# Performance work log

Measured on AMD Instinct MI355X. Metric: run time of the kernel, lower is better.

## Reference

```python
import jax, jax.numpy as jnp
import numpy as np

B, S, H = 2, 1024, 1024
NH, NKV, HD = 16, 4, 64
E, TOPK, I = 8, 2, 3584
EPS = 1e-5
THETA = 1e6


def setup_inputs() -> dict:
    key = jax.random.key(0)
    ks = jax.random.split(key, 12)
    def w(k, shape, fan_in):
        return jax.random.normal(k, shape, dtype=jnp.float32) * (1.0 / np.sqrt(fan_in))
    return {
        "hidden_states": jax.random.normal(ks[0], (B, S, H), dtype=jnp.float32),
        "position_ids": jnp.broadcast_to(jnp.arange(S, dtype=jnp.int64)[None, :], (B, S)),
        "ln1_w": jnp.ones((H,), jnp.float32),
        "ln2_w": jnp.ones((H,), jnp.float32),
        "wq": w(ks[1], (H, NH * HD), H),
        "wk": w(ks[2], (H, NKV * HD), H),
        "wv": w(ks[3], (H, NKV * HD), H),
        "wo": w(ks[4], (NH * HD, H), NH * HD),
        "router_w": w(ks[5], (H, E), H),
        "w_gate": w(ks[6], (E, H, I), H),
        "w_up": w(ks[7], (E, H, I), H),
        "w_down": w(ks[8], (E, I, H), I),
    }


def _rmsnorm(x, w):
    xf = x.astype(jnp.float32)
    return (xf * jax.lax.rsqrt(jnp.mean(xf * xf, -1, keepdims=True) + EPS)).astype(x.dtype) * w


def _rope(x, pos):
    # x: [B,S,nh,HD], pos: [B,S]
    inv_freq = 1.0 / (THETA ** (jnp.arange(0, HD, 2, dtype=jnp.float32) / HD))
    ang = pos.astype(jnp.float32)[..., None] * inv_freq            # [B,S,HD/2]
    emb = jnp.concatenate([ang, ang], axis=-1)                      # [B,S,HD]
    cos, sin = jnp.cos(emb)[:, :, None, :], jnp.sin(emb)[:, :, None, :]
    x1, x2 = x[..., : HD // 2], x[..., HD // 2:]
    rot = jnp.concatenate([-x2, x1], axis=-1)
    return x * cos + rot * sin


def _forward(hidden_states, position_ids, ln1_w, ln2_w, wq, wk, wv, wo,
             router_w, w_gate, w_up, w_down):
    residual = hidden_states
    x = _rmsnorm(hidden_states, ln1_w)

    # ---- attention (GQA, causal, RoPE) ----
    q = (x @ wq).reshape(B, S, NH, HD)
    k = (x @ wk).reshape(B, S, NKV, HD)
    v = (x @ wv).reshape(B, S, NKV, HD)
    q = _rope(q, position_ids)
    k = _rope(k, position_ids)
    rep = NH // NKV
    k = jnp.repeat(k, rep, axis=2)  # [B,S,NH,HD]
    v = jnp.repeat(v, rep, axis=2)
    scores = jnp.einsum("bqhd,bkhd->bhqk", q, k) / np.sqrt(HD)
    causal = jnp.tril(jnp.ones((S, S), bool))
    scores = jnp.where(causal[None, None], scores, jnp.finfo(scores.dtype).min)
    probs = jax.nn.softmax(scores, axis=-1)
    attn = jnp.einsum("bhqk,bkhd->bqhd", probs, v).reshape(B, S, NH * HD)
    hidden = residual + attn @ wo

    # ---- MoE MLP ----
    residual = hidden
    xn = _rmsnorm(hidden, ln2_w).reshape(-1, H)               # [T,H]
    T = xn.shape[0]
    logits = xn @ router_w                                    # [T,E]
    rprobs = jax.nn.softmax(logits.astype(jnp.float32), axis=-1)
    topv, topi = jax.lax.top_k(rprobs, TOPK)                  # [T,TOPK]
    topv = topv / jnp.sum(topv, axis=-1, keepdims=True)       # normalize_top_k_affinities
    weights = jnp.zeros((T, E), jnp.float32).at[jnp.arange(T)[:, None], topi].set(topv)
    g = jnp.einsum("th,ehi->eti", xn, w_gate)                 # [E,T,I]
    u = jnp.einsum("th,ehi->eti", xn, w_up)
    a = jax.nn.silu(g) * u
    eo = jnp.einsum("eti,eih->eth", a, w_down)                # [E,T,H]
    moe = jnp.einsum("eth,te->th", eo, weights).reshape(B, S, H)
    return residual + moe


def reference(hidden_states, position_ids, ln1_w, ln2_w, wq, wk, wv, wo,
              router_w, w_gate, w_up, w_down):
    return _forward(hidden_states, position_ids, ln1_w, ln2_w, wq, wk, wv, wo,
                    router_w, w_gate, w_up, w_down)
```

## Files before the change

### kernel.cpp

```cpp
#include <hip/hip_runtime.h>
#include <hip/hip_bf16.h>
#include <math.h>

#define Bc 2
#define Sc 1024
#define Hc 1024
#define NHc 16
#define NKVc 4
#define HDc 64
#define Ec 8
#define TOPKc 2
#define Ic 3584
#define Tc (Bc*Sc)
#define EPSc 1e-5f

typedef __attribute__((ext_vector_type(8))) short bf16x8;
typedef __attribute__((ext_vector_type(4))) float f32x4;

__device__ __forceinline__ unsigned short f2bf(float f) {
    union { float f; unsigned u; } v; v.f = f;
    unsigned r = v.u + 0x7fffu + ((v.u >> 16) & 1u);
    return (unsigned short)(r >> 16);
}

__device__ __forceinline__ unsigned cvt_pk_bf16(float lo, float hi) {
    unsigned r;
    asm("v_cvt_pk_bf16_f32 %0, %1, %2" : "=v"(r) : "v"(lo), "v"(hi));
    return r;
}

#define GLL(g, l) __builtin_amdgcn_global_load_lds( \
    (const __attribute__((address_space(1))) void*)(g), \
    (__attribute__((address_space(3))) void*)(l), 16, 0, 0)

static const size_t OFF_XN1  = 0;
static const size_t OFF_QB   = 8*1024*1024;
static const size_t OFF_KB   = OFF_QB + 8*1024*1024;
static const size_t OFF_VB   = OFF_KB + 2*1024*1024;
static const size_t OFF_XN2F = OFF_VB + 2*1024*1024;
static const size_t OFF_XN2B = OFF_XN2F + 8*1024*1024;
static const size_t OFF_ACT  = OFF_XN2B + 4*1024*1024;
static const size_t OFF_ROUTE= OFF_ACT + (size_t)4096*3584*2;

__global__ __launch_bounds__(256) void rmsnorm_kernel(const float* __restrict__ x,
        const float* __restrict__ w, float* __restrict__ outf,
        unsigned short* __restrict__ outb) {
    int t = blockIdx.x;
    int tid = threadIdx.x;
    const float* row = x + (size_t)t * Hc;
    float ss = 0.f;
    for (int h = tid; h < Hc; h += 256) { float v = row[h]; ss += v*v; }
    __shared__ float red[256];
    red[tid] = ss; __syncthreads();
    for (int s = 128; s > 0; s >>= 1) { if (tid < s) red[tid] += red[tid+s]; __syncthreads(); }
    float scale = rsqrtf(red[0] / (float)Hc + EPSc);
    for (int h = tid; h < Hc; h += 256) {
        float v = row[h] * scale * w[h];
        outf[(size_t)t*Hc + h] = v;
        if (outb) outb[(size_t)t*Hc + h] = f2bf(v);
    }
}

__global__ __launch_bounds__(256) void qkv_gemm(const float* __restrict__ A,
        const float* __restrict__ wq, const float* __restrict__ wk, const float* __restrict__ wv,
        float* __restrict__ qout, float* __restrict__ kout, float* __restrict__ vout) {
    __shared__ float As[64][17];
    __shared__ float Bs[16][65];
    int n0 = blockIdx.x * 64;
    int m0 = blockIdx.y * 64;
    int tid = threadIdx.x;
    int tx = tid & 15, ty = tid >> 4;
    const float* Bp; int ldb, c0;
    if (n0 < 1024)      { Bp = wq; ldb = 1024; c0 = n0; }
    else if (n0 < 1280) { Bp = wk; ldb = 256;  c0 = n0 - 1024; }
    else                { Bp = wv; ldb = 256;  c0 = n0 - 1280; }
    float acc[4][4] = {};
    for (int k0 = 0; k0 < 1024; k0 += 16) {
        #pragma unroll
        for (int i = 0; i < 4; i++) {
            int lin = tid + i*256; int r = lin >> 4, k = lin & 15;
            As[r][k] = A[(size_t)(m0 + r)*Hc + k0 + k];
        }
        #pragma unroll
        for (int i = 0; i < 4; i++) {
            int lin = tid + i*256; int r = lin >> 6, c = lin & 63;
            Bs[r][c] = Bp[(size_t)(k0 + r)*ldb + c0 + c];
        }
        __syncthreads();
        #pragma unroll
        for (int kk = 0; kk < 16; kk++) {
            float a[4], b[4];
            #pragma unroll
            for (int i = 0; i < 4; i++) a[i] = As[ty*4+i][kk];
            #pragma unroll
            for (int j = 0; j < 4; j++) b[j] = Bs[kk][tx*4+j];
            #pragma unroll
            for (int i = 0; i < 4; i++)
                #pragma unroll
                for (int j = 0; j < 4; j++) acc[i][j] += a[i]*b[j];
        }
        __syncthreads();
    }
    #pragma unroll
    for (int i = 0; i < 4; i++) {
        int m = m0 + ty*4 + i;
        #pragma unroll
        for (int j = 0; j < 4; j++) {
            int n = n0 + tx*4 + j;
            float val = acc[i][j];
            if (n < 1024)      qout[(size_t)m*1024 + n] = val;
            else if (n < 1280) kout[(size_t)m*256 + (n-1024)] = val;
            else               vout[(size_t)m*256 + (n-1280)] = val;
        }
    }
}

__global__ __launch_bounds__(256) void rope_kernel(float* __restrict__ q, float* __restrict__ k) {
    int idx = blockIdx.x*256 + threadIdx.x;
    const int total = Tc*(NHc+NKVc)*32;
    if (idx >= total) return;
    int d = idx & 31;
    int rest = idx >> 5;
    int head = rest % (NHc+NKVc);
    int t = rest / (NHc+NKVc);
    int s = t & (Sc-1);
    float inv = exp2f(-(float)d * 0.62286152f);
    float ang = (float)s * inv;
    float c = cosf(ang), sn = sinf(ang);
    float* base;
    if (head < NHc) base = q + (size_t)t*1024 + head*64;
    else            base = k + (size_t)t*256  + (head-NHc)*64;
    float x1 = base[d], x2 = base[d+32];
    base[d]    = x1*c - x2*sn;
    base[d+32] = x2*c + x1*sn;
}

__global__ __launch_bounds__(256) void attn_kernel(const float* __restrict__ q,
        const float* __restrict__ kbuf, const float* __restrict__ vbuf,
        float* __restrict__ attn) {
    __shared__ float Qs[64][65];
    __shared__ float KVs[64][65];
    __shared__ float Ps[64][65];
    __shared__ float m_s[64], l_s[64], al_s[64];
    int q0 = blockIdx.x * 64;
    int h  = blockIdx.y;
    int b  = blockIdx.z;
    int hk = h >> 2;
    int tid = threadIdx.x;
    int tx = tid & 15, ty = tid >> 4;
    #pragma unroll
    for (int i = 0; i < 16; i++) {
        int lin = tid + i*256; int r = lin >> 6, d = lin & 63;
        Qs[r][d] = q[((size_t)(b*Sc + q0 + r))*1024 + h*64 + d];
    }
    if (tid < 64) { m_s[tid] = -INFINITY; l_s[tid] = 0.f; }
    float O[4][4] = {};
    for (int j0 = 0; j0 <= q0; j0 += 64) {
        __syncthreads();
        #pragma unroll
        for (int i = 0; i < 16; i++) {
            int lin = tid + i*256; int r = lin >> 6, d = lin & 63;
            KVs[r][d] = kbuf[((size_t)(b*Sc + j0 + r))*256 + hk*64 + d];
        }
        __syncthreads();
        float sc[4][4] = {};
        for (int d = 0; d < 64; d++) {
            float a[4], bb[4];
            #pragma unroll
            for (int i = 0; i < 4; i++) a[i] = Qs[ty*4+i][d];
            #pragma unroll
            for (int j = 0; j < 4; j++) bb[j] = KVs[tx*4+j][d];
            #pragma unroll
            for (int i = 0; i < 4; i++)
                #pragma unroll
                for (int j = 0; j < 4; j++) sc[i][j] += a[i]*bb[j];
        }
        bool diag = (j0 == q0);
        #pragma unroll
        for (int i = 0; i < 4; i++) {
            int r = ty*4+i;
            #pragma unroll
            for (int j = 0; j < 4; j++) {
                int c = tx*4+j;
                float v = sc[i][j]*0.125f;
                if (diag && c > r) v = -1e30f;
                Ps[r][c] = v;
            }
        }
        __syncthreads();
        if (tid < 64) {
            int r = tid;
            float mx = -1e30f;
            for (int c = 0; c < 64; c++) mx = fmaxf(mx, Ps[r][c]);
            float newm = fmaxf(m_s[r], mx);
            float alpha = expf(m_s[r] - newm);
            float sum = 0.f;
            for (int c = 0; c < 64; c++) { float p = expf(Ps[r][c] - newm); Ps[r][c] = p; sum += p; }
            l_s[r] = l_s[r]*alpha + sum;
            m_s[r] = newm;
            al_s[r] = alpha;
        }
        #pragma unroll
        for (int i = 0; i < 16; i++) {
            int lin = tid + i*256; int r = lin >> 6, d = lin & 63;
            KVs[r][d] = vbuf[((size_t)(b*Sc + j0 + r))*256 + hk*64 + d];
        }
        __syncthreads();
        #pragma unroll
        for (int i = 0; i < 4; i++) {
            float al = al_s[ty*4+i];
            #pragma unroll
            for (int j = 0; j < 4; j++) O[i][j] *= al;
        }
        for (int c = 0; c < 64; c++) {
            float p[4], vv[4];
            #pragma unroll
            for (int i = 0; i < 4; i++) p[i] = Ps[ty*4+i][c];
            #pragma unroll
            for (int j = 0; j < 4; j++) vv[j] = KVs[c][tx*4+j];
            #pragma unroll
            for (int i = 0; i < 4; i++)
                #pragma unroll
                for (int j = 0; j < 4; j++) O[i][j] += p[i]*vv[j];
        }
    }
    #pragma unroll
    for (int i = 0; i < 4; i++) {
        int r = ty*4+i;
        float inv_l = 1.f / l_s[r];
        int m = b*Sc + q0 + r;
        #pragma unroll
        for (int j = 0; j < 4; j++) {
            int d = tx*4+j;
            attn[(size_t)m*1024 + h*64 + d] = O[i][j]*inv_l;
        }
    }
}

__global__ __launch_bounds__(256) void wo_gemm(const float* __restrict__ A,
        const float* __restrict__ wo, const float* __restrict__ resid,
        float* __restrict__ out) {
    __shared__ float As[64][17];
    __shared__ float Bs[16][65];
    int n0 = blockIdx.x * 64;
    int m0 = blockIdx.y * 64;
    int tid = threadIdx.x;
    int tx = tid & 15, ty = tid >> 4;
    float acc[4][4] = {};
    for (int k0 = 0; k0 < 1024; k0 += 16) {
        #pragma unroll
        for (int i = 0; i < 4; i++) {
            int lin = tid + i*256; int r = lin >> 4, k = lin & 15;
            As[r][k] = A[(size_t)(m0 + r)*Hc + k0 + k];
        }
        #pragma unroll
        for (int i = 0; i < 4; i++) {
            int lin = tid + i*256; int r = lin >> 6, c = lin & 63;
            Bs[r][c] = wo[(size_t)(k0 + r)*Hc + n0 + c];
        }
        __syncthreads();
        #pragma unroll
        for (int kk = 0; kk < 16; kk++) {
            float a[4], b[4];
            #pragma unroll
            for (int i = 0; i < 4; i++) a[i] = As[ty*4+i][kk];
            #pragma unroll
            for (int j = 0; j < 4; j++) b[j] = Bs[kk][tx*4+j];
            #pragma unroll
            for (int i = 0; i < 4; i++)
                #pragma unroll
                for (int j = 0; j < 4; j++) acc[i][j] += a[i]*b[j];
        }
        __syncthreads();
    }
    #pragma unroll
    for (int i = 0; i < 4; i++) {
        int m = m0 + ty*4 + i;
        #pragma unroll
        for (int j = 0; j < 4; j++) {
            int n = n0 + tx*4 + j;
            out[(size_t)m*Hc + n] = acc[i][j] + resid[(size_t)m*Hc + n];
        }
    }
}

__global__ __launch_bounds__(256) void router_kernel(const float* __restrict__ xn2,
        const float* __restrict__ rw, int* __restrict__ counts,
        int* __restrict__ topk_e, float* __restrict__ topk_w) {
    int t = blockIdx.x, tid = threadIdx.x;
    float part[8] = {};
    for (int h = tid; h < 1024; h += 256) {
        float x = xn2[(size_t)t*Hc + h];
        #pragma unroll
        for (int e = 0; e < 8; e++) part[e] += x * rw[h*8 + e];
    }
    __shared__ float red[8][256];
    #pragma unroll
    for (int e = 0; e < 8; e++) red[e][tid] = part[e];
    __syncthreads();
    for (int s = 128; s > 0; s >>= 1) {
        if (tid < s) {
            #pragma unroll
            for (int e = 0; e < 8; e++) red[e][tid] += red[e][tid+s];
        }
        __syncthreads();
    }
    if (tid == 0) {
        float lg[8]; float mx = -1e30f;
        for (int e = 0; e < 8; e++) { lg[e] = red[e][0]; mx = fmaxf(mx, lg[e]); }
        float p[8]; float sum = 0.f;
        for (int e = 0; e < 8; e++) { p[e] = expf(lg[e]-mx); sum += p[e]; }
        for (int e = 0; e < 8; e++) p[e] /= sum;
        int e0 = 0;
        for (int e = 1; e < 8; e++) if (p[e] > p[e0]) e0 = e;
        int e1 = -1;
        for (int e = 0; e < 8; e++) { if (e == e0) continue; if (e1 < 0 || p[e] > p[e1]) e1 = e; }
        float w0 = p[e0], w1 = p[e1]; float wsum = w0 + w1; w0 /= wsum; w1 /= wsum;
        topk_e[t*2] = e0; topk_e[t*2+1] = e1;
        topk_w[t*2] = w0; topk_w[t*2+1] = w1;
        atomicAdd(&counts[e0], 1); atomicAdd(&counts[e1], 1);
    }
}

__global__ void prefix_kernel(const int* __restrict__ counts, int* __restrict__ offsets) {
    if (threadIdx.x == 0 && blockIdx.x == 0) {
        int acc = 0;
        for (int e = 0; e < 8; e++) { offsets[e] = acc; acc += counts[e]; }
    }
}

__global__ __launch_bounds__(256) void fill_kernel(const int* __restrict__ topk_e,
        const float* __restrict__ topk_w, const int* __restrict__ offsets,
        int* __restrict__ fill, int* __restrict__ list_tok, float* __restrict__ list_w) {
    int t = blockIdx.x*256 + threadIdx.x;
    if (t >= Tc) return;
    #pragma unroll
    for (int j = 0; j < 2; j++) {
        int e = topk_e[t*2+j]; float w = topk_w[t*2+j];
        int slot = atomicAdd(&fill[e], 1);
        list_tok[offsets[e]+slot] = t;
        list_w[offsets[e]+slot] = w;
    }
}

__global__ __launch_bounds__(256) void gemm_gateup(const unsigned short* __restrict__ xn2b,
        const float* __restrict__ wg, const float* __restrict__ wu,
        const int* __restrict__ counts, const int* __restrict__ offsets,
        const int* __restrict__ list_tok, unsigned short* __restrict__ act) {
    int e = blockIdx.z;
    int cnt = counts[e];
    int m0 = blockIdx.y * 128;
    if (m0 >= cnt) return;
    int n0 = blockIdx.x * 64;
    int aoff = offsets[e];
    __shared__ alignas(16) unsigned short As[2][128*32];
    __shared__ alignas(16) float Bgs[2][32*64];
    __shared__ alignas(16) float Bus[2][32*64];
    __shared__ int toks[128];
    int tid = threadIdx.x;
    if (tid < 128) toks[tid] = list_tok[aoff + min(m0 + tid, cnt-1)];
    __syncthreads();
    const float* Bgp = wg + (size_t)e*Hc*Ic + n0;
    const float* Bup = wu + (size_t)e*Hc*Ic + n0;
    int lane = tid & 63, wave = tid >> 6;
    int wm = wave >> 1, wn = wave & 1;
    int ml = lane & 15, quad = lane >> 4;
    int wb = wave * 64;

    const unsigned short* aS0 = xn2b + (size_t)toks[tid>>2]*Hc + (tid&3)*8;
    const unsigned short* aS1 = xn2b + (size_t)toks[(tid+256)>>2]*Hc + (tid&3)*8;
    const float* gS0 = Bgp + (size_t)(tid>>4)*Ic + (tid&15)*4;
    const float* gS1 = Bgp + (size_t)((tid>>4)+16)*Ic + (tid&15)*4;
    const float* uS0 = Bup + (size_t)(tid>>4)*Ic + (tid&15)*4;
    const float* uS1 = Bup + (size_t)((tid>>4)+16)*Ic + (tid&15)*4;

    #define GU_STAGE(buf, K0) do { \
        GLL(aS0 + (K0), &As[buf][wb*8]); \
        GLL(aS1 + (K0), &As[buf][(256+wb)*8]); \
        GLL(gS0 + (size_t)(K0)*Ic, &Bgs[buf][wb*4]); \
        GLL(gS1 + (size_t)(K0)*Ic, &Bgs[buf][(256+wb)*4]); \
        GLL(uS0 + (size_t)(K0)*Ic, &Bus[buf][wb*4]); \
        GLL(uS1 + (size_t)(K0)*Ic, &Bus[buf][(256+wb)*4]); \
    } while(0)

    f32x4 accg[4][2] = {}, accu[4][2] = {};
    GU_STAGE(0, 0);
    asm volatile("s_waitcnt vmcnt(0)" ::: "memory");
    __syncthreads();
    int cur = 0;
    for (int ks = 0; ks < Hc/32; ks++) {
        if (ks + 1 < Hc/32) GU_STAGE(cur^1, (ks+1)*32);
        bf16x8 a[4];
        #pragma unroll
        for (int mt = 0; mt < 4; mt++) {
            int R = wm*64 + mt*16 + ml;
            a[mt] = *reinterpret_cast<const bf16x8*>(&As[cur][R*32 + quad*8]);
        }
        bf16x8 bg[2], bu[2];
        #pragma unroll
        for (int nt = 0; nt < 2; nt++) {
            int n = wn*32 + nt*16 + ml;
            const float* pg = &Bgs[cur][quad*512 + n];
            const float* pu = &Bus[cur][quad*512 + n];
            union { bf16x8 v; unsigned u[4]; } tg, tu;
            #pragma unroll
            for (int j = 0; j < 4; j++) {
                tg.u[j] = cvt_pk_bf16(pg[(2*j)*64], pg[(2*j+1)*64]);
                tu.u[j] = cvt_pk_bf16(pu[(2*j)*64], pu[(2*j+1)*64]);
            }
            bg[nt] = tg.v; bu[nt] = tu.v;
        }
        #pragma unroll
        for (int mt = 0; mt < 4; mt++)
            #pragma unroll
            for (int nt = 0; nt < 2; nt++) {
                accg[mt][nt] = __builtin_amdgcn_mfma_f32_16x16x32_bf16(a[mt], bg[nt], accg[mt][nt], 0, 0, 0);
                accu[mt][nt] = __builtin_amdgcn_mfma_f32_16x16x32_bf16(a[mt], bu[nt], accu[mt][nt], 0, 0, 0);
            }
        asm volatile("s_waitcnt vmcnt(0)" ::: "memory");
        __syncthreads();
        cur ^= 1;
    }
    #undef GU_STAGE
    #pragma unroll
    for (int mt = 0; mt < 4; mt++)
        #pragma unroll
        for (int nt = 0; nt < 2; nt++)
            #pragma unroll
            for (int rg = 0; rg < 4; rg++) {
                int rowl = wm*64 + mt*16 + quad*4 + rg;
                if (m0 + rowl < cnt) {
                    int n = n0 + wn*32 + nt*16 + ml;
                    float g = accg[mt][nt][rg], u = accu[mt][nt][rg];
                    float sg = g / (1.f + expf(-g));
                    act[(size_t)(aoff + m0 + rowl)*Ic + n] = f2bf(sg * u);
                }
            }
}

__global__ __launch_bounds__(256) void gemm_down(const unsigned short* __restrict__ act,
        const float* __restrict__ wd, const int* __restrict__ counts,
        const int* __restrict__ offsets, const int* __restrict__ list_tok,
        const float* __restrict__ list_w, float* __restrict__ out) {
    int e = blockIdx.z;
    int cnt = counts[e];
    int m0 = blockIdx.y * 128;
    if (m0 >= cnt) return;
    int n0 = blockIdx.x * 64;
    int aoff = offsets[e];
    __shared__ alignas(16) unsigned short As[2][128*32];
    __shared__ alignas(16) float Bs[2][32*64];
    const unsigned short* Aexp = act + (size_t)(aoff + m0)*Ic;
    const float* Bp = wd + (size_t)e*Ic*Hc + n0;
    int rowclamp = cnt - 1 - m0;
    int tid = threadIdx.x;
    int lane = tid & 63, wave = tid >> 6;
    int wm = wave >> 1, wn = wave & 1;
    int ml = lane & 15, quad = lane >> 4;
    int wb = wave * 64;

    int R0 = min(tid >> 2, rowclamp);
    int R1 = min((tid + 256) >> 2, rowclamp);
    const unsigned short* aS0 = Aexp + (size_t)R0*Ic + (tid&3)*8;
    const unsigned short* aS1 = Aexp + (size_t)R1*Ic + (tid&3)*8;
    const float* bS0 = Bp + (size_t)(tid>>4)*Hc + (tid&15)*4;
    const float* bS1 = Bp + (size_t)((tid>>4)+16)*Hc + (tid&15)*4;

    #define DN_STAGE(buf, K0) do { \
        GLL(aS0 + (K0), &As[buf][wb*8]); \
        GLL(aS1 + (K0), &As[buf][(256+wb)*8]); \
        GLL(bS0 + (size_t)(K0)*Hc, &Bs[buf][wb*4]); \
        GLL(bS1 + (size_t)(K0)*Hc, &Bs[buf][(256+wb)*4]); \
    } while(0)

    f32x4 acc[4][2] = {};
    DN_STAGE(0, 0);
    asm volatile("s_waitcnt vmcnt(0)" ::: "memory");
    __syncthreads();
    int cur = 0;
    for (int ks = 0; ks < Ic/32; ks++) {
        if (ks + 1 < Ic/32) DN_STAGE(cur^1, (ks+1)*32);
        bf16x8 a[4];
        #pragma unroll
        for (int mt = 0; mt < 4; mt++) {
            int R = wm*64 + mt*16 + ml;
            a[mt] = *reinterpret_cast<const bf16x8*>(&As[cur][R*32 + quad*8]);
        }
        bf16x8 b[2];
        #pragma unroll
        for (int nt = 0; nt < 2; nt++) {
            int n = wn*32 + nt*16 + ml;
            const float* pb = &Bs[cur][quad*512 + n];
            union { bf16x8 v; unsigned u[4]; } tb;
            #pragma unroll
            for (int j = 0; j < 4; j++)
                tb.u[j] = cvt_pk_bf16(pb[(2*j)*64], pb[(2*j+1)*64]);
            b[nt] = tb.v;
        }
        #pragma unroll
        for (int mt = 0; mt < 4; mt++)
            #pragma unroll
            for (int nt = 0; nt < 2; nt++)
                acc[mt][nt] = __builtin_amdgcn_mfma_f32_16x16x32_bf16(a[mt], b[nt], acc[mt][nt], 0, 0, 0);
        asm volatile("s_waitcnt vmcnt(0)" ::: "memory");
        __syncthreads();
        cur ^= 1;
    }
    #undef DN_STAGE
    #pragma unroll
    for (int mt = 0; mt < 4; mt++)
        #pragma unroll
        for (int nt = 0; nt < 2; nt++)
            #pragma unroll
            for (int rg = 0; rg < 4; rg++) {
                int rowl = wm*64 + mt*16 + quad*4 + rg;
                if (m0 + rowl < cnt) {
                    int t = list_tok[aoff + m0 + rowl];
                    float w = list_w[aoff + m0 + rowl];
                    int n = n0 + wn*32 + nt*16 + ml;
                    atomicAdd(&out[(size_t)t*Hc + n], w * acc[mt][nt][rg]);
                }
            }
}

extern "C" void kernel_launch(void* const* d_in, const int* in_sizes, int n_in,
                              void* d_out, int out_size, void* d_ws, size_t ws_size,
                              hipStream_t stream) {
    const float* hidden = (const float*)d_in[0];
    const float* ln1 = (const float*)d_in[2];
    const float* ln2 = (const float*)d_in[3];
    const float* wq  = (const float*)d_in[4];
    const float* wk  = (const float*)d_in[5];
    const float* wv  = (const float*)d_in[6];
    const float* wo  = (const float*)d_in[7];
    const float* rw  = (const float*)d_in[8];
    const float* wg  = (const float*)d_in[9];
    const float* wu  = (const float*)d_in[10];
    const float* wd  = (const float*)d_in[11];
    float* out = (float*)d_out;
    char* ws = (char*)d_ws;

    float* xn1f  = (float*)(ws + OFF_XN1);
    float* attnf = xn1f;
    float* qb    = (float*)(ws + OFF_QB);
    float* kb    = (float*)(ws + OFF_KB);
    float* vb    = (float*)(ws + OFF_VB);
    float* xn2f  = (float*)(ws + OFF_XN2F);
    unsigned short* xn2b = (unsigned short*)(ws + OFF_XN2B);
    unsigned short* act  = (unsigned short*)(ws + OFF_ACT);
    int*   route    = (int*)(ws + OFF_ROUTE);
    int*   counts   = route;
    int*   fillc    = route + 8;
    int*   offsets  = route + 16;
    int*   topk_e   = route + 24;
    float* topk_w   = (float*)(route + 24 + 2*Tc);
    int*   list_tok = route + 24 + 4*Tc;
    float* list_w   = (float*)(route + 24 + 6*Tc);

    hipMemsetAsync(counts, 0, 16*sizeof(int), stream);

    rmsnorm_kernel<<<Tc, 256, 0, stream>>>(hidden, ln1, xn1f, nullptr);
    qkv_gemm<<<dim3(24, 32), 256, 0, stream>>>(xn1f, wq, wk, wv, qb, kb, vb);
    rope_kernel<<<(Tc*(NHc+NKVc)*32 + 255)/256, 256, 0, stream>>>(qb, kb);
    attn_kernel<<<dim3(16, 16, 2), 256, 0, stream>>>(qb, kb, vb, attnf);
    wo_gemm<<<dim3(16, 32), 256, 0, stream>>>(attnf, wo, hidden, out);
    rmsnorm_kernel<<<Tc, 256, 0, stream>>>(out, ln2, xn2f, xn2b);
    router_kernel<<<Tc, 256, 0, stream>>>(xn2f, rw, counts, topk_e, topk_w);
    prefix_kernel<<<1, 64, 0, stream>>>(counts, offsets);
    fill_kernel<<<(Tc+255)/256, 256, 0, stream>>>(topk_e, topk_w, offsets, fillc, list_tok, list_w);
    gemm_gateup<<<dim3(56, 16, 8), 256, 0, stream>>>(xn2b, wg, wu, counts, offsets, list_tok, act);
    gemm_down<<<dim3(16, 16, 8), 256, 0, stream>>>(act, wd, counts, offsets, list_tok, list_w, out);
}
```

Baseline: 1.154 ms.

## Restructure attention kernel with register softmax, vectorized LDS, and fewer barriers

Rewrites the flash-attention tile loop. Q/K/V loads become 128-bit vector loads into padded shared memory, with a rotated K layout to avoid bank conflicts. The online softmax moves from a serial 64-thread pass over shared memory into registers, using cross-lane shuffles for row max and sum, and K and V are loaded together. This removes idle threads and several barriers per tile, at the cost of more shared memory (four 64x68 buffers) and more registers.

```diff
diff --git a/kernel.cpp b/kernel.cpp
--- a/kernel.cpp
+++ b/kernel.cpp
@@ -138,102 +138,126 @@
 __global__ __launch_bounds__(256) void attn_kernel(const float* __restrict__ q,
         const float* __restrict__ kbuf, const float* __restrict__ vbuf,
         float* __restrict__ attn) {
-    __shared__ float Qs[64][65];
-    __shared__ float KVs[64][65];
-    __shared__ float Ps[64][65];
-    __shared__ float m_s[64], l_s[64], al_s[64];
+    __shared__ alignas(16) float Qs[64][68];
+    __shared__ alignas(16) float Ks[64][68];
+    __shared__ alignas(16) float Vs[64][68];
+    __shared__ alignas(16) float Ps[64][68];
     int q0 = blockIdx.x * 64;
     int h  = blockIdx.y;
     int b  = blockIdx.z;
     int hk = h >> 2;
     int tid = threadIdx.x;
     int tx = tid & 15, ty = tid >> 4;
-    #pragma unroll
-    for (int i = 0; i < 16; i++) {
-        int lin = tid + i*256; int r = lin >> 6, d = lin & 63;
-        Qs[r][d] = q[((size_t)(b*Sc + q0 + r))*1024 + h*64 + d];
-    }
-    if (tid < 64) { m_s[tid] = -INFINITY; l_s[tid] = 0.f; }
-    float O[4][4] = {};
+
+    #pragma unroll
+    for (int it = 0; it < 4; it++) {
+        int s = tid + it*256;
+        int r = s >> 4, c4 = s & 15;
+        *reinterpret_cast<f32x4*>(&Qs[r][c4*4]) =
+            *reinterpret_cast<const f32x4*>(&q[((size_t)(b*Sc + q0 + r))*1024 + h*64 + c4*4]);
+    }
+
+    float m_reg[4], l_reg[4];
+    #pragma unroll
+    for (int i = 0; i < 4; i++) { m_reg[i] = -INFINITY; l_reg[i] = 0.f; }
+    f32x4 O[4] = {};
+    int rotk = tx & 7;
+
     for (int j0 = 0; j0 <= q0; j0 += 64) {
-        __syncthreads();
-        #pragma unroll
-        for (int i = 0; i < 16; i++) {
-            int lin = tid + i*256; int r = lin >> 6, d = lin & 63;
-            KVs[r][d] = kbuf[((size_t)(b*Sc + j0 + r))*256 + hk*64 + d];
-        }
-        __syncthreads();
-        float sc[4][4] = {};
-        for (int d = 0; d < 64; d++) {
-            float a[4], bb[4];
-            #pragma unroll
-            for (int i = 0; i < 4; i++) a[i] = Qs[ty*4+i][d];
-            #pragma unroll
-            for (int j = 0; j < 4; j++) bb[j] = KVs[tx*4+j][d];
+        #pragma unroll
+        for (int it = 0; it < 4; it++) {
+            int s = tid + it*256;
+            int r = s >> 4, c4 = s & 15;
+            int rot = (s >> 6) & 7;
+            size_t grow = ((size_t)(b*Sc + j0 + r))*256 + hk*64 + c4*4;
+            *reinterpret_cast<f32x4*>(&Ks[r][((c4 + rot) & 15)*4]) =
+                *reinterpret_cast<const f32x4*>(&kbuf[grow]);
+            *reinterpret_cast<f32x4*>(&Vs[r][c4*4]) =
+                *reinterpret_cast<const f32x4*>(&vbuf[grow]);
+        }
+        __syncthreads();
+
+        f32x4 sc[4] = {};
+        for (int d0 = 0; d0 < 16; d0++) {
+            f32x4 a[4], bb[4];
+            #pragma unroll
+            for (int i = 0; i < 4; i++)
+                a[i] = *reinterpret_cast<const f32x4*>(&Qs[ty*4+i][d0*4]);
+            int ck = ((d0 + rotk) & 15) * 4;
+            #pragma unroll
+            for (int j = 0; j < 4; j++)
+                bb[j] = *reinterpret_cast<const f32x4*>(&Ks[tx*4+j][ck]);
             #pragma unroll
             for (int i = 0; i < 4; i++)
                 #pragma unroll
-                for (int j = 0; j < 4; j++) sc[i][j] += a[i]*bb[j];
-        }
+                for (int j = 0; j < 4; j++)
+                    sc[i][j] += a[i][0]*bb[j][0] + a[i][1]*bb[j][1]
+                              + a[i][2]*bb[j][2] + a[i][3]*bb[j][3];
+        }
+
         bool diag = (j0 == q0);
         #pragma unroll
         for (int i = 0; i < 4; i++) {
-            int r = ty*4+i;
+            int r = ty*4 + i;
+            float mx = -1e30f;
             #pragma unroll
             for (int j = 0; j < 4; j++) {
-                int c = tx*4+j;
                 float v = sc[i][j]*0.125f;
-                if (diag && c > r) v = -1e30f;
-                Ps[r][c] = v;
+                if (diag && (tx*4+j) > r) v = -1e30f;
+                sc[i][j] = v;
+                mx = fmaxf(mx, v);
             }
-        }
-        __syncthreads();
-        if (tid < 64) {
-            int r = tid;
-            float mx = -1e30f;
-            for (int c = 0; c < 64; c++) mx = fmaxf(mx, Ps[r][c]);
-            float newm = fmaxf(m_s[r], mx);
-            float alpha = expf(m_s[r] - newm);
+            mx = fmaxf(mx, __shfl_xor(mx, 1));
+            mx = fmaxf(mx, __shfl_xor(mx, 2));
+            mx = fmaxf(mx, __shfl_xor(mx, 4));
+            mx = fmaxf(mx, __shfl_xor(mx, 8));
+            float nm = fmaxf(m_reg[i], mx);
+            float alpha = __expf(m_reg[i] - nm);
+            m_reg[i] = nm;
             float sum = 0.f;
-            for (int c = 0; c < 64; c++) { float p = expf(Ps[r][c] - newm); Ps[r][c] = p; sum += p; }
-            l_s[r] = l_s[r]*alpha + sum;
-            m_s[r] = newm;
-            al_s[r] = alpha;
-        }
-        #pragma unroll
-        for (int i = 0; i < 16; i++) {
-            int lin = tid + i*256; int r = lin >> 6, d = lin & 63;
-            KVs[r][d] = vbuf[((size_t)(b*Sc + j0 + r))*256 + hk*64 + d];
-        }
-        __syncthreads();
-        #pragma unroll
-        for (int i = 0; i < 4; i++) {
-            float al = al_s[ty*4+i];
-            #pragma unroll
-            for (int j = 0; j < 4; j++) O[i][j] *= al;
-        }
-        for (int c = 0; c < 64; c++) {
-            float p[4], vv[4];
-            #pragma unroll
-            for (int i = 0; i < 4; i++) p[i] = Ps[ty*4+i][c];
-            #pragma unroll
-            for (int j = 0; j < 4; j++) vv[j] = KVs[c][tx*4+j];
+            #pragma unroll
+            for (int j = 0; j < 4; j++) {
+                float p = __expf(sc[i][j] - nm);
+                sc[i][j] = p;
+                sum += p;
+            }
+            sum += __shfl_xor(sum, 1);
+            sum += __shfl_xor(sum, 2);
+            sum += __shfl_xor(sum, 4);
+            sum += __shfl_xor(sum, 8);
+            l_reg[i] = l_reg[i]*alpha + sum;
+            #pragma unroll
+            for (int j = 0; j < 4; j++) O[i][j] *= alpha;
+            *reinterpret_cast<f32x4*>(&Ps[r][tx*4]) = sc[i];
+        }
+        __syncthreads();
+
+        for (int c0 = 0; c0 < 16; c0++) {
+            f32x4 p4[4], v4[4];
+            #pragma unroll
+            for (int i = 0; i < 4; i++)
+                p4[i] = *reinterpret_cast<const f32x4*>(&Ps[ty*4+i][c0*4]);
+            #pragma unroll
+            for (int cj = 0; cj < 4; cj++)
+                v4[cj] = *reinterpret_cast<const f32x4*>(&Vs[c0*4+cj][tx*4]);
             #pragma unroll
             for (int i = 0; i < 4; i++)
                 #pragma unroll
-                for (int j = 0; j < 4; j++) O[i][j] += p[i]*vv[j];
-        }
-    }
+                for (int j = 0; j < 4; j++)
+                    O[i][j] += p4[i][0]*v4[0][j] + p4[i][1]*v4[1][j]
+                             + p4[i][2]*v4[2][j] + p4[i][3]*v4[3][j];
+        }
+        __syncthreads();
+    }
+
     #pragma unroll
     for (int i = 0; i < 4; i++) {
-        int r = ty*4+i;
-        float inv_l = 1.f / l_s[r];
+        int r = ty*4 + i;
+        float inv_l = 1.f / l_reg[i];
         int m = b*Sc + q0 + r;
-        #pragma unroll
-        for (int j = 0; j < 4; j++) {
-            int d = tx*4+j;
-            attn[(size_t)m*1024 + h*64 + d] = O[i][j]*inv_l;
-        }
+        f32x4 o = O[i];
+        o[0] *= inv_l; o[1] *= inv_l; o[2] *= inv_l; o[3] *= inv_l;
+        *reinterpret_cast<f32x4*>(&attn[(size_t)m*1024 + h*64 + tx*4]) = o;
     }
 }
 
```

New measurement: 1.183 ms. 1.03x slower.
